# Performance work log

Measured on AMD Instinct MI355X. Metric: run time of the kernel, lower is better.

Reference implementation:

```python
import jax, jax.numpy as jnp
import numpy as np

B, L, D, NL = 4, 4096, 1024, 8921
INIT_STD = 0.03


def setup_inputs() -> dict:
    key = jax.random.key(0)
    kx, k1, k2 = jax.random.split(key, 3)
    x = jax.random.normal(kx, (B, L, D), dtype=jnp.float32)
    W1 = jax.random.normal(k1, (D, D), dtype=jnp.float32) * INIT_STD  # l1_linear.weight
    W2 = jax.random.normal(k2, (NL, D), dtype=jnp.float32) * INIT_STD  # l2_linear.weight
    return {"x": x, "W1": W1, "W2": W2}


def reference(x, W1, W2):
    # l1_output = tanh(x @ W1^T)                        [B, L, D]
    l1 = jnp.tanh(jnp.einsum("bld,ed->ble", x, W1))
    # scores = l1 @ W2^T                                [B, L, NL]
    scores = jnp.einsum("bld,nd->bln", l1, W2)
    # softmax over sequence dim (dim=1), then transpose -> [B, NL, L]
    attn = jax.nn.softmax(scores, axis=1).transpose(0, 2, 1)
    # attention_output = attn @ x                       [B, NL, D]
    out = jnp.einsum("bnl,bld->bnd", attn, x)
    return (out, attn)
```

## Files before the change

kernel.cpp:

```cpp
#include <hip/hip_runtime.h>
#include <math.h>

#define B_ 4
#define L_ 4096
#define D_ 1024
#define NL_ 8921
#define NLP_ 8960

typedef __bf16 bf16;
typedef bf16 bf16x8 __attribute__((ext_vector_type(8)));
typedef bf16 bf16x4 __attribute__((ext_vector_type(4)));
typedef float f32x4 __attribute__((ext_vector_type(4)));

__device__ __forceinline__ void async_ld16(const void* g, void* l) {
  __builtin_amdgcn_global_load_lds(
      (__attribute__((address_space(1))) const unsigned int*)g,
      (__attribute__((address_space(3))) unsigned int*)l, 16, 0, 0);
}


__global__ __launch_bounds__(256) void convx_kernel(const float* __restrict__ x,
                                                    bf16* __restrict__ xb,
                                                    bf16* __restrict__ xbT) {
  __shared__ bf16 t[64][65];
  int b = blockIdx.z;
  int l0 = blockIdx.y * 64, d0 = blockIdx.x * 64;
  int tx = threadIdx.x & 63, ty = threadIdx.x >> 6;
  const float* xp = x + (size_t)b * L_ * D_;
  bf16* xbp = xb + (size_t)b * L_ * D_;
#pragma unroll
  for (int i = 0; i < 16; ++i) {
    int l = ty + i * 4;
    float v = xp[(size_t)(l0 + l) * D_ + d0 + tx];
    bf16 bv = (bf16)v;
    xbp[(size_t)(l0 + l) * D_ + d0 + tx] = bv;
    t[l][tx] = bv;
  }
  __syncthreads();
  bf16* xtp = xbT + (size_t)b * D_ * L_;
#pragma unroll
  for (int i = 0; i < 16; ++i) {
    int d = ty + i * 4;
    xtp[(size_t)(d0 + d) * L_ + l0 + tx] = t[tx][d];
  }
}

__global__ __launch_bounds__(256) void convw1_kernel(const float* __restrict__ W,
                                                     bf16* __restrict__ Wb) {
  int i = (blockIdx.x * 256 + threadIdx.x) * 4;
  f32x4 v = *(const f32x4*)(W + i);
  bf16x4 o;
  o[0] = (bf16)v[0]; o[1] = (bf16)v[1]; o[2] = (bf16)v[2]; o[3] = (bf16)v[3];
  *(bf16x4*)(Wb + i) = o;
}

__global__ __launch_bounds__(256) void convw2_kernel(const float* __restrict__ W2,
                                                     bf16* __restrict__ w2b) {
  int i = (blockIdx.x * 256 + threadIdx.x) * 4;
  int n = i >> 10;
  bf16x4 o;
  if (n < NL_) {
    f32x4 v = *(const f32x4*)(W2 + (size_t)i);
    o[0] = (bf16)v[0]; o[1] = (bf16)v[1]; o[2] = (bf16)v[2]; o[3] = (bf16)v[3];
  } else {
    o[0] = o[1] = o[2] = o[3] = (bf16)0.0f;
  }
  *(bf16x4*)(w2b + i) = o;
}

__global__ __launch_bounds__(256) void gemm1_kernel(const bf16* __restrict__ A,
                                                    const bf16* __restrict__ Bm,
                                                    bf16* __restrict__ C) {
  __shared__ bf16 sA[128 * 64];
  __shared__ bf16 sB[128 * 64];
  int tid = threadIdx.x;
  int wave = tid >> 6, lane = tid & 63;
  int wr = wave >> 1, wc = wave & 1;
  int row0 = blockIdx.y * 128, col0 = blockIdx.x * 128;
  int lm = lane & 15, lk = (lane >> 4) * 8, quad = lane >> 4;
  f32x4 acc[4][4];
#pragma unroll
  for (int i = 0; i < 4; ++i)
#pragma unroll
    for (int j = 0; j < 4; ++j)
#pragma unroll
      for (int r = 0; r < 4; ++r) acc[i][j][r] = 0.f;

  for (int k0 = 0; k0 < D_; k0 += 64) {
#pragma unroll
    for (int j = 0; j < 4; ++j) {
      int e = j * 2048 + wave * 512 + lane * 8;
      int r = e >> 6, kk = e & 63;
      async_ld16(A + (size_t)(row0 + r) * D_ + k0 + kk, (char*)sA + j * 4096 + wave * 1024);
      async_ld16(Bm + (size_t)(col0 + r) * D_ + k0 + kk, (char*)sB + j * 4096 + wave * 1024);
    }
    __syncthreads();
#pragma unroll
    for (int kc = 0; kc < 2; ++kc) {
      bf16x8 af[4], bfr[4];
#pragma unroll
      for (int i = 0; i < 4; ++i)
        af[i] = *(const bf16x8*)(sA + (wr * 64 + i * 16 + lm) * 64 + kc * 32 + lk);
#pragma unroll
      for (int j = 0; j < 4; ++j)
        bfr[j] = *(const bf16x8*)(sB + (wc * 64 + j * 16 + lm) * 64 + kc * 32 + lk);
#pragma unroll
      for (int i = 0; i < 4; ++i)
#pragma unroll
        for (int j = 0; j < 4; ++j)
          acc[i][j] = __builtin_amdgcn_mfma_f32_16x16x32_bf16(af[i], bfr[j], acc[i][j], 0, 0, 0);
    }
    __syncthreads();
  }
#pragma unroll
  for (int i = 0; i < 4; ++i)
#pragma unroll
    for (int j = 0; j < 4; ++j)
#pragma unroll
      for (int r = 0; r < 4; ++r) {
        int row = row0 + wr * 64 + i * 16 + quad * 4 + r;
        int col = col0 + wc * 64 + j * 16 + lm;
        C[(size_t)row * D_ + col] = (bf16)tanhf(acc[i][j][r]);
      }
}

__global__ __launch_bounds__(256) void gemm2_kernel(const bf16* __restrict__ A,
                                                    const bf16* __restrict__ Bm,
                                                    float* __restrict__ attn) {
  __shared__ bf16 sA[128 * 64];
  __shared__ bf16 sB[128 * 64];
  int tid = threadIdx.x;
  int wave = tid >> 6, lane = tid & 63;
  int wr = wave >> 1, wc = wave & 1;
  int row0 = blockIdx.y * 128, col0 = blockIdx.x * 128;
  int lm = lane & 15, lk = (lane >> 4) * 8, quad = lane >> 4;
  f32x4 acc[4][4];
#pragma unroll
  for (int i = 0; i < 4; ++i)
#pragma unroll
    for (int j = 0; j < 4; ++j)
#pragma unroll
      for (int r = 0; r < 4; ++r) acc[i][j][r] = 0.f;

  for (int k0 = 0; k0 < D_; k0 += 64) {
#pragma unroll
    for (int j = 0; j < 4; ++j) {
      int e = j * 2048 + wave * 512 + lane * 8;
      int r = e >> 6, kk = e & 63;
      async_ld16(A + (size_t)(row0 + r) * D_ + k0 + kk, (char*)sA + j * 4096 + wave * 1024);
      async_ld16(Bm + (size_t)(col0 + r) * D_ + k0 + kk, (char*)sB + j * 4096 + wave * 1024);
    }
    __syncthreads();
#pragma unroll
    for (int kc = 0; kc < 2; ++kc) {
      bf16x8 af[4], bfr[4];
#pragma unroll
      for (int i = 0; i < 4; ++i)
        af[i] = *(const bf16x8*)(sA + (wr * 64 + i * 16 + lm) * 64 + kc * 32 + lk);
#pragma unroll
      for (int j = 0; j < 4; ++j)
        bfr[j] = *(const bf16x8*)(sB + (wc * 64 + j * 16 + lm) * 64 + kc * 32 + lk);
#pragma unroll
      for (int i = 0; i < 4; ++i)
#pragma unroll
        for (int j = 0; j < 4; ++j)
          acc[i][j] = __builtin_amdgcn_mfma_f32_16x16x32_bf16(af[i], bfr[j], acc[i][j], 0, 0, 0);
    }
    __syncthreads();
  }
#pragma unroll
  for (int i = 0; i < 4; ++i)
#pragma unroll
    for (int j = 0; j < 4; ++j)
#pragma unroll
      for (int r = 0; r < 4; ++r) {
        int n = row0 + wr * 64 + i * 16 + quad * 4 + r;
        int col = col0 + wc * 64 + j * 16 + lm;
        if (n < NL_) {
          int b = col >> 12, l = col & 4095;
          attn[((size_t)b * NL_ + n) * L_ + l] = acc[i][j][r];
        }
      }
}

__global__ __launch_bounds__(256) void softmax_kernel(float* __restrict__ attn) {
  __shared__ float red[8];
  size_t row = blockIdx.x;
  float* p = attn + row * (size_t)L_;
  int tid = threadIdx.x;
  int lane = tid & 63, wave = tid >> 6;
  f32x4 v[4];
  float mx = -3.4e38f;
#pragma unroll
  for (int i = 0; i < 4; ++i) {
    v[i] = *(const f32x4*)(p + i * 1024 + tid * 4);
#pragma unroll
    for (int j = 0; j < 4; ++j) mx = fmaxf(mx, v[i][j]);
  }
#pragma unroll
  for (int o = 32; o > 0; o >>= 1) mx = fmaxf(mx, __shfl_xor(mx, o));
  if (lane == 0) red[wave] = mx;
  __syncthreads();
  mx = fmaxf(fmaxf(red[0], red[1]), fmaxf(red[2], red[3]));
  float sum = 0.f;
#pragma unroll
  for (int i = 0; i < 4; ++i)
#pragma unroll
    for (int j = 0; j < 4; ++j) {
      float e = __expf(v[i][j] - mx);
      v[i][j] = e;
      sum += e;
    }
#pragma unroll
  for (int o = 32; o > 0; o >>= 1) sum += __shfl_xor(sum, o);
  if (lane == 0) red[4 + wave] = sum;
  __syncthreads();
  sum = red[4] + red[5] + red[6] + red[7];
  float inv = 1.0f / sum;
#pragma unroll
  for (int i = 0; i < 4; ++i) {
    f32x4 o4 = v[i];
    o4[0] *= inv; o4[1] *= inv; o4[2] *= inv; o4[3] *= inv;
    *(f32x4*)(p + i * 1024 + tid * 4) = o4;
  }
}

__global__ __launch_bounds__(256) void gemm3_kernel(const float* __restrict__ attn,
                                                    const bf16* __restrict__ xbT,
                                                    float* __restrict__ out) {
  __shared__ bf16 sA[128 * 64];
  __shared__ bf16 sB[128 * 64];
  int tid = threadIdx.x;
  int wave = tid >> 6, lane = tid & 63;
  int wr = wave >> 1, wc = wave & 1;
  int b = blockIdx.z;
  int row0 = blockIdx.y * 128, col0 = blockIdx.x * 128;
  const float* Ab = attn + (size_t)b * NL_ * L_;
  const bf16* Bb = xbT + (size_t)b * D_ * L_;
  int lm = lane & 15, lk = (lane >> 4) * 8, quad = lane >> 4;
  f32x4 acc[4][4];
#pragma unroll
  for (int i = 0; i < 4; ++i)
#pragma unroll
    for (int j = 0; j < 4; ++j)
#pragma unroll
      for (int r = 0; r < 4; ++r) acc[i][j][r] = 0.f;

  for (int k0 = 0; k0 < L_; k0 += 64) {
#pragma unroll
    for (int j = 0; j < 4; ++j) {
      int e = j * 2048 + wave * 512 + lane * 8;
      int r = e >> 6, kk = e & 63;
      async_ld16(Bb + (size_t)(col0 + r) * L_ + k0 + kk, (char*)sB + j * 4096 + wave * 1024);
    }
#pragma unroll
    for (int t = 0; t < 8; ++t) {
      int e = t * 1024 + tid * 4;
      int r = e >> 6, kk = e & 63;
      int gr = row0 + r;
      gr = gr < NL_ ? gr : (NL_ - 1);
      f32x4 v = *(const f32x4*)(Ab + (size_t)gr * L_ + k0 + kk);
      bf16x4 o;
      o[0] = (bf16)v[0]; o[1] = (bf16)v[1]; o[2] = (bf16)v[2]; o[3] = (bf16)v[3];
      *(bf16x4*)(sA + e) = o;
    }
    __syncthreads();
#pragma unroll
    for (int kc = 0; kc < 2; ++kc) {
      bf16x8 af[4], bfr[4];
#pragma unroll
      for (int i = 0; i < 4; ++i)
        af[i] = *(const bf16x8*)(sA + (wr * 64 + i * 16 + lm) * 64 + kc * 32 + lk);
#pragma unroll
      for (int j = 0; j < 4; ++j)
        bfr[j] = *(const bf16x8*)(sB + (wc * 64 + j * 16 + lm) * 64 + kc * 32 + lk);
#pragma unroll
      for (int i = 0; i < 4; ++i)
#pragma unroll
        for (int j = 0; j < 4; ++j)
          acc[i][j] = __builtin_amdgcn_mfma_f32_16x16x32_bf16(af[i], bfr[j], acc[i][j], 0, 0, 0);
    }
    __syncthreads();
  }
#pragma unroll
  for (int i = 0; i < 4; ++i)
#pragma unroll
    for (int j = 0; j < 4; ++j)
#pragma unroll
      for (int r = 0; r < 4; ++r) {
        int n = row0 + wr * 64 + i * 16 + quad * 4 + r;
        int d = col0 + wc * 64 + j * 16 + lm;
        if (n < NL_) out[((size_t)b * NL_ + n) * D_ + d] = acc[i][j][r];
      }
}

extern "C" void kernel_launch(void* const* d_in, const int* in_sizes, int n_in,
                              void* d_out, int out_size, void* d_ws, size_t ws_size,
                              hipStream_t stream) {
  const float* x = (const float*)d_in[0];
  const float* W1 = (const float*)d_in[1];
  const float* W2 = (const float*)d_in[2];
  float* out = (float*)d_out;
  float* attn = out + (size_t)B_ * NL_ * D_;

  char* ws = (char*)d_ws;
  bf16* xb = (bf16*)(ws);
  bf16* xbT = (bf16*)(ws + 33554432);
  bf16* w1b = (bf16*)(ws + 67108864);
  bf16* w2b = (bf16*)(ws + 69206016);
  bf16* l1b = (bf16*)(ws + 87556096);

  convx_kernel<<<dim3(D_ / 64, L_ / 64, B_), 256, 0, stream>>>(x, xb, xbT);
  convw1_kernel<<<(D_ * D_) / 1024, 256, 0, stream>>>(W1, w1b);
  convw2_kernel<<<(NLP_ * D_) / 1024, 256, 0, stream>>>(W2, w2b);

  gemm1_kernel<<<dim3(D_ / 128, (B_ * L_) / 128), 256, 0, stream>>>(xb, w1b, l1b);
  gemm2_kernel<<<dim3((B_ * L_) / 128, NLP_ / 128), 256, 0, stream>>>(w2b, l1b, attn);
  softmax_kernel<<<B_ * NL_, 256, 0, stream>>>(attn);
  gemm3_kernel<<<dim3(D_ / 128, NLP_ / 128, B_), 256, 0, stream>>>(attn, xbT, out);
}
```

Before: 2.145 ms.

## Emit bf16 attention copy from softmax and remap GEMM block order for XCDs

The softmax kernel now also writes a bf16 copy of the attention matrix into workspace when space allows. gemm3 can then load A tiles with async global-to-LDS loads instead of reading fp32 and converting in registers, halving A-side read traffic. Both gemm2 and gemm3 remap the flat block index so consecutive tiles land on the same XCD (stride-8 interleave), aiming for better L2 reuse. The cost is an extra bf16 write of the full attention matrix (about 290MB) and a dependence on workspace size.

New measurement: 1.993 ms. 7.1% less time.

```diff
diff --git a/kernel.cpp b/kernel.cpp
--- a/kernel.cpp
+++ b/kernel.cpp
@@ -132,7 +132,10 @@
   int tid = threadIdx.x;
   int wave = tid >> 6, lane = tid & 63;
   int wr = wave >> 1, wc = wave & 1;
-  int row0 = blockIdx.y * 128, col0 = blockIdx.x * 128;
+  int flat = blockIdx.x + (blockIdx.y << 7);
+  int id = (flat & 7) * 1120 + (flat >> 3);
+  int row0 = (id >> 7) * 128;
+  int col0 = (id & 127) * 128;
   int lm = lane & 15, lk = (lane >> 4) * 8, quad = lane >> 4;
   f32x4 acc[4][4];
 #pragma unroll
@@ -183,7 +186,8 @@
       }
 }
 
-__global__ __launch_bounds__(256) void softmax_kernel(float* __restrict__ attn) {
+__global__ __launch_bounds__(256) void softmax_kernel(float* __restrict__ attn,
+                                                      bf16* __restrict__ attnb) {
   __shared__ float red[8];
   size_t row = blockIdx.x;
   float* p = attn + row * (size_t)L_;
@@ -217,15 +221,23 @@
   __syncthreads();
   sum = red[4] + red[5] + red[6] + red[7];
   float inv = 1.0f / sum;
+  bf16* q = attnb ? attnb + row * (size_t)L_ : (bf16*)0;
 #pragma unroll
   for (int i = 0; i < 4; ++i) {
     f32x4 o4 = v[i];
     o4[0] *= inv; o4[1] *= inv; o4[2] *= inv; o4[3] *= inv;
     *(f32x4*)(p + i * 1024 + tid * 4) = o4;
-  }
-}
-
-__global__ __launch_bounds__(256) void gemm3_kernel(const float* __restrict__ attn,
+    if (q) {
+      bf16x4 ob;
+      ob[0] = (bf16)o4[0]; ob[1] = (bf16)o4[1];
+      ob[2] = (bf16)o4[2]; ob[3] = (bf16)o4[3];
+      *(bf16x4*)(q + i * 1024 + tid * 4) = ob;
+    }
+  }
+}
+
+template <int ABF16>
+__global__ __launch_bounds__(256) void gemm3_kernel(const void* __restrict__ Ap,
                                                     const bf16* __restrict__ xbT,
                                                     float* __restrict__ out) {
   __shared__ bf16 sA[128 * 64];
@@ -233,9 +245,12 @@
   int tid = threadIdx.x;
   int wave = tid >> 6, lane = tid & 63;
   int wr = wave >> 1, wc = wave & 1;
-  int b = blockIdx.z;
-  int row0 = blockIdx.y * 128, col0 = blockIdx.x * 128;
-  const float* Ab = attn + (size_t)b * NL_ * L_;
+  int flat = blockIdx.x + (blockIdx.y << 3) + blockIdx.z * 560;
+  int id = (flat & 7) * 280 + (flat >> 3);
+  int col0 = (id & 7) * 128;
+  int yz = id >> 3;
+  int b = yz / 70;
+  int row0 = (yz - b * 70) * 128;
   const bf16* Bb = xbT + (size_t)b * D_ * L_;
   int lm = lane & 15, lk = (lane >> 4) * 8, quad = lane >> 4;
   f32x4 acc[4][4];
@@ -253,16 +268,29 @@
       int r = e >> 6, kk = e & 63;
       async_ld16(Bb + (size_t)(col0 + r) * L_ + k0 + kk, (char*)sB + j * 4096 + wave * 1024);
     }
-#pragma unroll
-    for (int t = 0; t < 8; ++t) {
-      int e = t * 1024 + tid * 4;
-      int r = e >> 6, kk = e & 63;
-      int gr = row0 + r;
-      gr = gr < NL_ ? gr : (NL_ - 1);
-      f32x4 v = *(const f32x4*)(Ab + (size_t)gr * L_ + k0 + kk);
-      bf16x4 o;
-      o[0] = (bf16)v[0]; o[1] = (bf16)v[1]; o[2] = (bf16)v[2]; o[3] = (bf16)v[3];
-      *(bf16x4*)(sA + e) = o;
+    if constexpr (ABF16) {
+      const bf16* Ab = (const bf16*)Ap + (size_t)b * NL_ * L_;
+#pragma unroll
+      for (int j = 0; j < 4; ++j) {
+        int e = j * 2048 + wave * 512 + lane * 8;
+        int r = e >> 6, kk = e & 63;
+        int gr = row0 + r;
+        gr = gr < NL_ ? gr : (NL_ - 1);
+        async_ld16(Ab + (size_t)gr * L_ + k0 + kk, (char*)sA + j * 4096 + wave * 1024);
+      }
+    } else {
+      const float* Ab = (const float*)Ap + (size_t)b * NL_ * L_;
+#pragma unroll
+      for (int u = 0; u < 8; ++u) {
+        int e = u * 1024 + tid * 4;
+        int r = e >> 6, kk = e & 63;
+        int gr = row0 + r;
+        gr = gr < NL_ ? gr : (NL_ - 1);
+        f32x4 v = *(const f32x4*)(Ab + (size_t)gr * L_ + k0 + kk);
+        bf16x4 o;
+        o[0] = (bf16)v[0]; o[1] = (bf16)v[1]; o[2] = (bf16)v[2]; o[3] = (bf16)v[3];
+        *(bf16x4*)(sA + e) = o;
+      }
     }
     __syncthreads();
 #pragma unroll
@@ -309,6 +337,8 @@
   bf16* w1b = (bf16*)(ws + 67108864);
   bf16* w2b = (bf16*)(ws + 69206016);
   bf16* l1b = (bf16*)(ws + 87556096);
+  size_t need = 121110528ULL + (size_t)B_ * NL_ * L_ * 2;
+  bf16* attnb = (ws_size >= need) ? (bf16*)(ws + 121110528) : (bf16*)0;
 
   convx_kernel<<<dim3(D_ / 64, L_ / 64, B_), 256, 0, stream>>>(x, xb, xbT);
   convw1_kernel<<<(D_ * D_) / 1024, 256, 0, stream>>>(W1, w1b);
@@ -316,6 +346,9 @@
 
   gemm1_kernel<<<dim3(D_ / 128, (B_ * L_) / 128), 256, 0, stream>>>(xb, w1b, l1b);
   gemm2_kernel<<<dim3((B_ * L_) / 128, NLP_ / 128), 256, 0, stream>>>(w2b, l1b, attn);
-  softmax_kernel<<<B_ * NL_, 256, 0, stream>>>(attn);
-  gemm3_kernel<<<dim3(D_ / 128, NLP_ / 128, B_), 256, 0, stream>>>(attn, xbT, out);
-}
+  softmax_kernel<<<B_ * NL_, 256, 0, stream>>>(attn, attnb);
+  if (attnb)
+    gemm3_kernel<1><<<dim3(D_ / 128, NLP_ / 128, B_), 256, 0, stream>>>(attnb, xbT, out);
+  else
+    gemm3_kernel<0><<<dim3(D_ / 128, NLP_ / 128, B_), 256, 0, stream>>>(attn, xbT, out);
+}
```
